# Kernel tuning notes

Hardware: AMD Instinct MI355X
Metric: run time of the kernel (lower is better)

Reference implementation:

```python
import jax, jax.numpy as jnp
import numpy as np

B = 16          # number of point clouds
N_COARSE = 1024  # points per cloud at coarse level
N_FINE = 4096    # points per cloud at fine level
C_IN = 256       # coarse feature channels
C_SKIP = 128     # fine skip feature channels
C_HID = 256
EPS = 1e-16


def setup_inputs() -> dict:
    key = jax.random.key(0)
    ks = jax.random.split(key, 8)
    x = jax.random.normal(ks[0], (B * N_COARSE, C_IN), dtype=jnp.float32)
    pos = jax.random.uniform(ks[1], (B * N_COARSE, 3), dtype=jnp.float32)
    x_skip = jax.random.normal(ks[2], (B * N_FINE, C_SKIP), dtype=jnp.float32)
    pos_skip = jax.random.uniform(ks[3], (B * N_FINE, 3), dtype=jnp.float32)
    # uniform batch assignment (sorted), one segment per cloud
    batch = jnp.repeat(jnp.arange(B, dtype=jnp.int32), N_COARSE)
    batch_skip = jnp.repeat(jnp.arange(B, dtype=jnp.int32), N_FINE)
    # MLP params: Linear(384 -> 256) + ReLU, Linear(256 -> 256) + ReLU
    c0 = C_IN + C_SKIP
    W1 = jax.random.normal(ks[4], (c0, C_HID), dtype=jnp.float32) / np.sqrt(c0)
    b1 = jnp.zeros((C_HID,), dtype=jnp.float32)
    W2 = jax.random.normal(ks[5], (C_HID, C_HID), dtype=jnp.float32) / np.sqrt(C_HID)
    b2 = jnp.zeros((C_HID,), dtype=jnp.float32)
    return {"x": x, "pos": pos, "x_skip": x_skip, "pos_skip": pos_skip,
            "W1": W1, "b1": b1, "W2": W2, "b2": b2,
            "batch": batch, "batch_skip": batch_skip, "k": 3}


def _knn_interpolate(x, pos, pos_skip, k):
    # batch is uniform: reshape into [B, n, ...] blocks (same as per-batch kNN)
    xb = x.reshape(B, N_COARSE, -1)          # [B, Nc, C]
    pc = pos.reshape(B, N_COARSE, 3)         # [B, Nc, 3]
    pf = pos_skip.reshape(B, N_FINE, 3)      # [B, Nf, 3]
    # squared pairwise distances within each cloud: [B, Nf, Nc]
    d2 = jnp.sum((pf[:, :, None, :] - pc[:, None, :, :]) ** 2, axis=-1)
    neg_d2, idx = jax.lax.top_k(-d2, k)      # k nearest -> [B, Nf, k]
    w = 1.0 / jnp.maximum(-neg_d2, EPS)      # inverse-squared-distance weights
    gathered = jax.vmap(lambda xc, i: xc[i])(xb, idx)  # [B, Nf, k, C]
    interp = jnp.sum(w[..., None] * gathered, axis=2) / jnp.sum(w, axis=2, keepdims=True)
    return interp.reshape(B * N_FINE, -1)    # [B*Nf, C]


def reference(x, pos, x_skip, pos_skip, W1, b1, W2, b2, batch, batch_skip, k):
    x_up = _knn_interpolate(x, pos, pos_skip, k)
    h = jnp.concatenate([x_up, x_skip], axis=1)          # [B*Nf, C_IN+C_SKIP]
    h = jax.nn.relu(h @ W1 + b1)
    h = jax.nn.relu(h @ W2 + b2)
    return (h, pos_skip, batch_skip)
```

## Files before the change

### kernel.cpp

```cpp
#include <hip/hip_runtime.h>

#define B_ 16
#define NC 1024
#define NF 4096
#define CIN 256
#define CSKIP 128
#define CHID 256
#define MTOT (B_ * NF)
#define EPS_ 1e-16f

typedef _Float16 f16;
typedef __attribute__((ext_vector_type(8))) _Float16 f16x8;
typedef __attribute__((ext_vector_type(4))) _Float16 f16x4;
typedef __attribute__((ext_vector_type(4))) float f32x4;


__device__ __forceinline__ void gload16(const void* g, void* l)
{
    __builtin_amdgcn_global_load_lds(
        (const __attribute__((address_space(1))) unsigned int*)g,
        (__attribute__((address_space(3))) unsigned int*)l, 16, 0, 0);
}

__global__ __launch_bounds__(256, 4) void misc_kernel(
    const float* __restrict__ x,
    const float* __restrict__ pos, const float* __restrict__ pos_skip,
    const int* __restrict__ batch_skip,
    const float* __restrict__ W1, const float* __restrict__ W2,
    const float* __restrict__ b1,
    int* __restrict__ idx3, float* __restrict__ w3,
    f16* __restrict__ W1bT, f16* __restrict__ W2T, float* __restrict__ b1p,
    f16* __restrict__ y, float* __restrict__ out_tail)
{
    __shared__ __align__(16) char smem[32768];
    const int bid = blockIdx.x;

    if (bid < 256) {
        f16* As = (f16*)smem;
        f16* Bs = (f16*)(smem + 16384);
        const int m0 = (bid >> 1) * 128;
        const int n0 = (bid & 1) * 128;
        const int tid  = threadIdx.x;
        const int lane = tid & 63;
        const int wid  = tid >> 6;
        const int wr   = wid >> 1, wc = wid & 1;
        const int srow = tid >> 1;
        const int scg  = tid & 1;
        const int bn4  = (tid & 31) << 2;
        const int bkb  = (tid >> 5) << 3;

        f32x4 acc[4][4] = {};
        for (int k0 = 0; k0 < 256; k0 += 64) {
            {
                const float* p = x + (size_t)(m0 + srow) * 256 + k0 + scg * 32;
                float v[32];
#pragma unroll
                for (int j = 0; j < 8; ++j) {
                    float4 a = ((const float4*)p)[j];
                    v[j*4+0]=a.x; v[j*4+1]=a.y; v[j*4+2]=a.z; v[j*4+3]=a.w;
                }
#pragma unroll
                for (int j = 0; j < 4; ++j) {
                    f16x8 hh;
#pragma unroll
                    for (int t2 = 0; t2 < 8; ++t2) hh[t2] = (f16)v[j*8+t2];
                    const int sphys = (scg*4 + j) ^ (srow & 7);
                    *(f16x8*)((char*)As + srow*128 + sphys*16) = hh;
                }
            }
#pragma unroll
            for (int c = 0; c < 2; ++c) {
                const int k = bkb + c * 4;
                const float* wp = W1 + (size_t)(k0 + k) * 256 + n0 + bn4;
                float4 r0 = *(const float4*)(wp);
                float4 r1 = *(const float4*)(wp + 256);
                float4 r2 = *(const float4*)(wp + 512);
                float4 r3 = *(const float4*)(wp + 768);
                const int half  = (k >> 2) & 1;
                const int kslot = k >> 3;
                f16x4 t0, t1, t2v, t3;
                t0[0]=(f16)r0.x; t0[1]=(f16)r1.x; t0[2]=(f16)r2.x; t0[3]=(f16)r3.x;
                t1[0]=(f16)r0.y; t1[1]=(f16)r1.y; t1[2]=(f16)r2.y; t1[3]=(f16)r3.y;
                t2v[0]=(f16)r0.z; t2v[1]=(f16)r1.z; t2v[2]=(f16)r2.z; t2v[3]=(f16)r3.z;
                t3[0]=(f16)r0.w; t3[1]=(f16)r1.w; t3[2]=(f16)r2.w; t3[3]=(f16)r3.w;
                *(f16x4*)((char*)Bs + (bn4+0)*128 + ((kslot ^ ((bn4+0)&7))*16) + half*8) = t0;
                *(f16x4*)((char*)Bs + (bn4+1)*128 + ((kslot ^ ((bn4+1)&7))*16) + half*8) = t1;
                *(f16x4*)((char*)Bs + (bn4+2)*128 + ((kslot ^ ((bn4+2)&7))*16) + half*8) = t2v;
                *(f16x4*)((char*)Bs + (bn4+3)*128 + ((kslot ^ ((bn4+3)&7))*16) + half*8) = t3;
            }
            __syncthreads();
#pragma unroll
            for (int h = 0; h < 2; ++h) {
                f16x8 aF[4], bF[4];
#pragma unroll
                for (int m = 0; m < 4; ++m) {
                    const int row  = wr*64 + m*16 + (lane & 15);
                    const int kg   = (h<<2) + (lane>>4);
                    const int slot = kg ^ (row & 7);
                    aF[m] = *(const f16x8*)((const char*)As + row*128 + slot*16);
                }
#pragma unroll
                for (int n = 0; n < 4; ++n) {
                    const int row  = wc*64 + n*16 + (lane & 15);
                    const int kg   = (h<<2) + (lane>>4);
                    const int slot = kg ^ (row & 7);
                    bF[n] = *(const f16x8*)((const char*)Bs + row*128 + slot*16);
                }
#pragma unroll
                for (int m = 0; m < 4; ++m)
#pragma unroll
                    for (int n = 0; n < 4; ++n)
                        acc[m][n] = __builtin_amdgcn_mfma_f32_16x16x32_f16(
                            aF[m], bF[n], acc[m][n], 0, 0, 0);
            }
            __syncthreads();
        }
        const int qq = lane & 15;
#pragma unroll
        for (int m = 0; m < 4; ++m) {
            const int rb = wr*64 + m*16 + ((lane>>4) << 2);
#pragma unroll
            for (int r = 0; r < 4; ++r) {
                const int rg = m0 + rb + r;
                f16x4 hv;
#pragma unroll
                for (int n = 0; n < 4; ++n) hv[n] = (f16)acc[m][n][r];
                *(f16x4*)&y[(size_t)rg * 256 + n0 + wc*64 + qq*4] = hv;
            }
        }
    } else if (bid < 2304) {
        float4* cpos = (float4*)smem;
        float*  cd   = (float*)(smem + 16384);
        int*    ci   = (int*)(smem + 19456);
        const int kb = bid - 256;
        const int b  = kb >> 7;
        const int fb = kb & 127;
        const float* cp = pos + (size_t)b * NC * 3;
        for (int i = threadIdx.x; i < NC; i += 256)
            cpos[i] = make_float4(cp[i*3], cp[i*3+1], cp[i*3+2], 0.0f);
        __syncthreads();

        const int fl = threadIdx.x & 31;
        const int q  = threadIdx.x >> 5;
        const int f  = b * NF + fb * 32 + fl;
        const float px = pos_skip[f*3+0];
        const float py = pos_skip[f*3+1];
        const float pz = pos_skip[f*3+2];

        float d0 = 3.4e38f, d1 = 3.4e38f, d2 = 3.4e38f;
        int   i0 = 0, i1 = 0, i2 = 0;
        const int jbase = q << 7;
#pragma unroll 4
        for (int jj = 0; jj < 128; ++jj) {
            const int j = jbase + jj;
            float4 c = cpos[j];
            float dx = px - c.x, dy = py - c.y, dz = pz - c.z;
            float d = fmaf(dx, dx, fmaf(dy, dy, dz * dz));
            const bool c2 = d < d2, c1 = d < d1, c0 = d < d0;
            d2 = c1 ? d1 : (c2 ? d : d2);  i2 = c1 ? i1 : (c2 ? j : i2);
            d1 = c0 ? d0 : (c1 ? d : d1);  i1 = c0 ? i0 : (c1 ? j : i1);
            d0 = c0 ? d  : d0;             i0 = c0 ? j  : i0;
        }
        const int cb = fl * 24 + q * 3;
        cd[cb+0] = d0; cd[cb+1] = d1; cd[cb+2] = d2;
        ci[cb+0] = i0; ci[cb+1] = i1; ci[cb+2] = i2;
        __syncthreads();

        if (threadIdx.x < 32) {
            float e0 = 3.4e38f, e1 = 3.4e38f, e2 = 3.4e38f;
            int   j0 = 0, j1 = 0, j2 = 0;
#pragma unroll
            for (int s = 0; s < 24; ++s) {
                const float d = cd[fl*24 + s];
                const int   j = ci[fl*24 + s];
                const bool c2 = d < e2, c1 = d < e1, c0 = d < e0;
                e2 = c1 ? e1 : (c2 ? d : e2);  j2 = c1 ? j1 : (c2 ? j : j2);
                e1 = c0 ? e0 : (c1 ? d : e1);  j1 = c0 ? j0 : (c1 ? j : j1);
                e0 = c0 ? d  : e0;             j0 = c0 ? j  : j0;
            }
            const float w0 = 1.0f / fmaxf(e0, EPS_);
            const float w1 = 1.0f / fmaxf(e1, EPS_);
            const float w2 = 1.0f / fmaxf(e2, EPS_);
            const float inv = 1.0f / (w0 + w1 + w2);
            idx3[f*3+0] = b * NC + j0;
            idx3[f*3+1] = b * NC + j1;
            idx3[f*3+2] = b * NC + j2;
            w3[f*3+0] = w0 * inv;
            w3[f*3+1] = w1 * inv;
            w3[f*3+2] = w2 * inv;
        }
    } else if (bid < 2689) {
        const int t = (bid - 2304) * 256 + threadIdx.x;
        if (t < 128 * 256) {
            const int k = t >> 8, n = t & 255;
            W1bT[n * 128 + k] = (f16)W1[(256 + k) * 256 + n];
        } else if (t < 128 * 256 + 256 * 256) {
            const int u = t - 128 * 256;
            const int n = u >> 8, j = u & 255;
            const int k = (j & ~63) + ((j & 3) << 4) + ((j >> 2) & 15);
            W2T[n * 256 + j] = (f16)W2[k * 256 + n];
        } else if (t < 128 * 256 + 256 * 256 + 256) {
            const int j = t - (128 * 256 + 256 * 256);
            const int k = (j & ~63) + ((j & 3) << 4) + ((j >> 2) & 15);
            b1p[j] = b1[k];
        }
    } else {
        const int i = (bid - 2689) * 256 + threadIdx.x;
        const int npos = MTOT * 3;
        if (i < npos)               out_tail[i] = pos_skip[i];
        else if (i < npos + MTOT)   out_tail[i] = (float)batch_skip[i - npos];
    }
}

__global__ __launch_bounds__(256, 2) void fused_gemm12(
    const float* __restrict__ A,
    const f16* __restrict__ B1t,
    const f16* __restrict__ y,
    const int* __restrict__ idx3, const float* __restrict__ w3,
    const float* __restrict__ b1p,
    const f16* __restrict__ B2t,
    const float* __restrict__ b2,
    float* __restrict__ out)
{
    __shared__ __align__(16) char lds[65536];
    f16*  Bs  = (f16*)lds;
    f16*  As  = (f16*)(lds + 32768);
    char* h1s = lds + 32768;

    const int tid  = threadIdx.x;
    const int lane = tid & 63;
    const int wid  = tid >> 6;
    const int wr   = wid >> 1, wc = wid & 1;
    const int m0   = blockIdx.x * 64;

    const int srow_l = lane >> 3;
    const int kch    = (lane & 7) ^ ((lane >> 3) & 7);

    f32x4 acc[2][8] = {};
    for (int k0 = 0; k0 < 128; k0 += 64) {
#pragma unroll
        for (int r = 0; r < 8; ++r) {
            const int c = (wid << 3) + r;
            const int row = (c << 3) + srow_l;
            gload16(B1t + (size_t)row * 128 + k0 + kch * 8, (char*)Bs + (c << 10));
        }
        {
            const int arow = tid >> 2, acg = tid & 3;
            const float* p = A + (size_t)(m0 + arow) * 128 + k0 + acg * 16;
            float v[16];
#pragma unroll
            for (int j = 0; j < 4; ++j) {
                float4 a = ((const float4*)p)[j];
                v[j*4+0]=a.x; v[j*4+1]=a.y; v[j*4+2]=a.z; v[j*4+3]=a.w;
            }
#pragma unroll
            for (int j = 0; j < 2; ++j) {
                f16x8 hh;
#pragma unroll
                for (int t2 = 0; t2 < 8; ++t2) hh[t2] = (f16)v[j*8+t2];
                const int sphys = (acg*2 + j) ^ (arow & 7);
                *(f16x8*)((char*)As + arow*128 + sphys*16) = hh;
            }
        }
        __syncthreads();
#pragma unroll
        for (int h = 0; h < 2; ++h) {
            f16x8 aF[2];
#pragma unroll
            for (int m = 0; m < 2; ++m) {
                const int row  = wr*32 + m*16 + (lane & 15);
                const int kg   = (h<<2) + (lane>>4);
                const int slot = kg ^ (row & 7);
                aF[m] = *(const f16x8*)((const char*)As + row*128 + slot*16);
            }
#pragma unroll
            for (int n = 0; n < 8; ++n) {
                const int row  = wc*128 + n*16 + (lane & 15);
                const int kg   = (h<<2) + (lane>>4);
                const int slot = kg ^ (row & 7);
                f16x8 bF = *(const f16x8*)((const char*)Bs + row*128 + slot*16);
#pragma unroll
                for (int m = 0; m < 2; ++m)
                    acc[m][n] = __builtin_amdgcn_mfma_f32_16x16x32_f16(
                        aF[m], bF, acc[m][n], 0, 0, 0);
            }
        }
        __syncthreads();
    }

    const int qq = lane & 15;
    const f32x4 bv0 = *(const f32x4*)&b1p[wc*128 + qq*4];
    const f32x4 bv1 = *(const f32x4*)&b1p[wc*128 + 64 + qq*4];
#pragma unroll
    for (int m = 0; m < 2; ++m) {
        const int rb = wr*32 + m*16 + ((lane>>4) << 2);
#pragma unroll
        for (int r = 0; r < 4; ++r) {
            const int rl = rb + r;
            const int rg = m0 + rl;
            const int i0 = idx3[rg*3+0], i1 = idx3[rg*3+1], i2 = idx3[rg*3+2];
            const float w0 = w3[rg*3+0], w1 = w3[rg*3+1], w2 = w3[rg*3+2];
#pragma unroll
            for (int g = 0; g < 2; ++g) {
                const int jb = wc*128 + g*64 + qq*4;
                f16x4 y0 = *(const f16x4*)&y[(size_t)i0 * 256 + jb];
                f16x4 y1 = *(const f16x4*)&y[(size_t)i1 * 256 + jb];
                f16x4 y2 = *(const f16x4*)&y[(size_t)i2 * 256 + jb];
                const f32x4 bv = g ? bv1 : bv0;
                f16x4 hv;
#pragma unroll
                for (int n = 0; n < 4; ++n) {
                    float v = acc[m][g*4+n][r]
                            + w0*(float)y0[n] + w1*(float)y1[n] + w2*(float)y2[n]
                            + bv[n];
                    hv[n] = (f16)fmaxf(v, 0.0f);
                }
                const int slot = jb >> 3;
                const int phys = (slot & ~7) | ((slot & 7) ^ (rl & 7));
                *(f16x4*)(h1s + rl*512 + phys*16 + ((jb >> 2) & 1) * 8) = hv;
            }
        }
    }
    __syncthreads();

    f32x4 acc2[2][8] = {};
    for (int k0 = 0; k0 < 256; k0 += 64) {
#pragma unroll
        for (int r = 0; r < 8; ++r) {
            const int c = (wid << 3) + r;
            const int row = (c << 3) + srow_l;
            gload16(B2t + (size_t)row * 256 + k0 + kch * 8, (char*)Bs + (c << 10));
        }
        __syncthreads();
#pragma unroll
        for (int h = 0; h < 2; ++h) {
            f16x8 aF[2];
#pragma unroll
            for (int m = 0; m < 2; ++m) {
                const int row   = wr*32 + m*16 + (lane & 15);
                const int kg    = (h<<2) + (lane>>4);
                const int aslot = (k0 >> 3) + (kg ^ (row & 7));
                aF[m] = *(const f16x8*)(h1s + row*512 + aslot*16);
            }
#pragma unroll
            for (int n = 0; n < 8; ++n) {
                const int row  = wc*128 + n*16 + (lane & 15);
                const int kg   = (h<<2) + (lane>>4);
                const int slot = kg ^ (row & 7);
                f16x8 bF = *(const f16x8*)((const char*)Bs + row*128 + slot*16);
#pragma unroll
                for (int m = 0; m < 2; ++m)
                    acc2[m][n] = __builtin_amdgcn_mfma_f32_16x16x32_f16(
                        aF[m], bF, acc2[m][n], 0, 0, 0);
            }
        }
        __syncthreads();
    }

#pragma unroll
    for (int m = 0; m < 2; ++m) {
#pragma unroll
        for (int n = 0; n < 8; ++n) {
            const int col = wc*128 + n*16 + (lane & 15);
            const float bv = b2[col];
#pragma unroll
            for (int r = 0; r < 4; ++r) {
                const int row = m0 + wr*32 + m*16 + ((lane>>4) << 2) + r;
                out[(size_t)row * 256 + col] = fmaxf(acc2[m][n][r] + bv, 0.0f);
            }
        }
    }
}

extern "C" void kernel_launch(void* const* d_in, const int* in_sizes, int n_in,
                              void* d_out, int out_size, void* d_ws, size_t ws_size,
                              hipStream_t stream)
{
    const float* x        = (const float*)d_in[0];
    const float* pos      = (const float*)d_in[1];
    const float* x_skip   = (const float*)d_in[2];
    const float* pos_skip = (const float*)d_in[3];
    const float* W1       = (const float*)d_in[4];
    const float* b1       = (const float*)d_in[5];
    const float* W2       = (const float*)d_in[6];
    const float* b2       = (const float*)d_in[7];
    const int*   batch_skip = (const int*)d_in[9];
    float* out = (float*)d_out;

    char* ws = (char*)d_ws;
    int*   idx3 = (int*)ws;
    float* w3   = (float*)(ws + (1u << 20));
    f16*   W1bT = (f16*)(ws + (2u << 20));
    f16*   W2T  = (f16*)(ws + (2u << 20) + (256u << 10));
    float* b1p  = (float*)(ws + (2u << 20) + (512u << 10));
    f16*   y    = (f16*)(ws + (4u << 20));

    misc_kernel<<<3713, 256, 0, stream>>>(
        x, pos, pos_skip, batch_skip, W1, W2, b1,
        idx3, w3, W1bT, W2T, b1p, y, out + (size_t)MTOT * CHID);

    fused_gemm12<<<MTOT / 64, 256, 0, stream>>>(
        x_skip, W1bT, y, idx3, w3, b1p, W2T, b2, out);
}
```

Measured before the change: 177.7 us.

## Move kNN search into the fused GEMM kernel and keep indices/weights in LDS

The kNN search leaves the preprocessing kernel and now runs at the start of each 64-row GEMM block. Four threads per fine point each scan 256 coarse points, and their partial top-3 lists are merged with wave shuffles. Indices and weights stay in LDS, so the idx3/w3 global round trip and 2048 blocks of work in the first kernel go away. In exchange the GEMM kernel does serial distance work before its MFMA phase, and LDS use grows slightly past 64KB, which may lower occupancy.

```diff
diff --git a/kernel.cpp b/kernel.cpp
--- a/kernel.cpp
+++ b/kernel.cpp
@@ -24,11 +24,9 @@
 
 __global__ __launch_bounds__(256, 4) void misc_kernel(
     const float* __restrict__ x,
-    const float* __restrict__ pos, const float* __restrict__ pos_skip,
-    const int* __restrict__ batch_skip,
+    const float* __restrict__ pos_skip, const int* __restrict__ batch_skip,
     const float* __restrict__ W1, const float* __restrict__ W2,
     const float* __restrict__ b1,
-    int* __restrict__ idx3, float* __restrict__ w3,
     f16* __restrict__ W1bT, f16* __restrict__ W2T, float* __restrict__ b1p,
     f16* __restrict__ y, float* __restrict__ out_tail)
 {
@@ -128,69 +126,8 @@
                 *(f16x4*)&y[(size_t)rg * 256 + n0 + wc*64 + qq*4] = hv;
             }
         }
-    } else if (bid < 2304) {
-        float4* cpos = (float4*)smem;
-        float*  cd   = (float*)(smem + 16384);
-        int*    ci   = (int*)(smem + 19456);
-        const int kb = bid - 256;
-        const int b  = kb >> 7;
-        const int fb = kb & 127;
-        const float* cp = pos + (size_t)b * NC * 3;
-        for (int i = threadIdx.x; i < NC; i += 256)
-            cpos[i] = make_float4(cp[i*3], cp[i*3+1], cp[i*3+2], 0.0f);
-        __syncthreads();
-
-        const int fl = threadIdx.x & 31;
-        const int q  = threadIdx.x >> 5;
-        const int f  = b * NF + fb * 32 + fl;
-        const float px = pos_skip[f*3+0];
-        const float py = pos_skip[f*3+1];
-        const float pz = pos_skip[f*3+2];
-
-        float d0 = 3.4e38f, d1 = 3.4e38f, d2 = 3.4e38f;
-        int   i0 = 0, i1 = 0, i2 = 0;
-        const int jbase = q << 7;
-#pragma unroll 4
-        for (int jj = 0; jj < 128; ++jj) {
-            const int j = jbase + jj;
-            float4 c = cpos[j];
-            float dx = px - c.x, dy = py - c.y, dz = pz - c.z;
-            float d = fmaf(dx, dx, fmaf(dy, dy, dz * dz));
-            const bool c2 = d < d2, c1 = d < d1, c0 = d < d0;
-            d2 = c1 ? d1 : (c2 ? d : d2);  i2 = c1 ? i1 : (c2 ? j : i2);
-            d1 = c0 ? d0 : (c1 ? d : d1);  i1 = c0 ? i0 : (c1 ? j : i1);
-            d0 = c0 ? d  : d0;             i0 = c0 ? j  : i0;
-        }
-        const int cb = fl * 24 + q * 3;
-        cd[cb+0] = d0; cd[cb+1] = d1; cd[cb+2] = d2;
-        ci[cb+0] = i0; ci[cb+1] = i1; ci[cb+2] = i2;
-        __syncthreads();
-
-        if (threadIdx.x < 32) {
-            float e0 = 3.4e38f, e1 = 3.4e38f, e2 = 3.4e38f;
-            int   j0 = 0, j1 = 0, j2 = 0;
-#pragma unroll
-            for (int s = 0; s < 24; ++s) {
-                const float d = cd[fl*24 + s];
-                const int   j = ci[fl*24 + s];
-                const bool c2 = d < e2, c1 = d < e1, c0 = d < e0;
-                e2 = c1 ? e1 : (c2 ? d : e2);  j2 = c1 ? j1 : (c2 ? j : j2);
-                e1 = c0 ? e0 : (c1 ? d : e1);  j1 = c0 ? j0 : (c1 ? j : j1);
-                e0 = c0 ? d  : e0;             j0 = c0 ? j  : j0;
-            }
-            const float w0 = 1.0f / fmaxf(e0, EPS_);
-            const float w1 = 1.0f / fmaxf(e1, EPS_);
-            const float w2 = 1.0f / fmaxf(e2, EPS_);
-            const float inv = 1.0f / (w0 + w1 + w2);
-            idx3[f*3+0] = b * NC + j0;
-            idx3[f*3+1] = b * NC + j1;
-            idx3[f*3+2] = b * NC + j2;
-            w3[f*3+0] = w0 * inv;
-            w3[f*3+1] = w1 * inv;
-            w3[f*3+2] = w2 * inv;
-        }
-    } else if (bid < 2689) {
-        const int t = (bid - 2304) * 256 + threadIdx.x;
+    } else if (bid < 641) {
+        const int t = (bid - 256) * 256 + threadIdx.x;
         if (t < 128 * 256) {
             const int k = t >> 8, n = t & 255;
             W1bT[n * 128 + k] = (f16)W1[(256 + k) * 256 + n];
@@ -205,33 +142,89 @@
             b1p[j] = b1[k];
         }
     } else {
-        const int i = (bid - 2689) * 256 + threadIdx.x;
+        const int i = (bid - 641) * 256 + threadIdx.x;
         const int npos = MTOT * 3;
         if (i < npos)               out_tail[i] = pos_skip[i];
         else if (i < npos + MTOT)   out_tail[i] = (float)batch_skip[i - npos];
     }
 }
 
-__global__ __launch_bounds__(256, 2) void fused_gemm12(
+__global__ __launch_bounds__(256, 2) void fused_all(
+    const float* __restrict__ pos, const float* __restrict__ pos_skip,
     const float* __restrict__ A,
     const f16* __restrict__ B1t,
     const f16* __restrict__ y,
-    const int* __restrict__ idx3, const float* __restrict__ w3,
     const float* __restrict__ b1p,
     const f16* __restrict__ B2t,
     const float* __restrict__ b2,
     float* __restrict__ out)
 {
-    __shared__ __align__(16) char lds[65536];
-    f16*  Bs  = (f16*)lds;
-    f16*  As  = (f16*)(lds + 32768);
-    char* h1s = lds + 32768;
+    __shared__ __align__(16) char lds[67072];
+    f16*   Bs  = (f16*)lds;
+    f16*   As  = (f16*)(lds + 32768);
+    char*  h1s = lds + 32768;
+    int*   kni = (int*)(lds + 65536);
+    float* knw = (float*)(lds + 65536 + 768);
 
     const int tid  = threadIdx.x;
     const int lane = tid & 63;
     const int wid  = tid >> 6;
     const int wr   = wid >> 1, wc = wid & 1;
     const int m0   = blockIdx.x * 64;
+    const int bat  = m0 >> 12;
+
+    {
+        float4* cpos = (float4*)(lds + 32768);
+        const float* cp = pos + (size_t)(bat << 10) * 3;
+        for (int i = tid; i < NC; i += 256)
+            cpos[i] = make_float4(cp[i*3], cp[i*3+1], cp[i*3+2], 0.0f);
+        __syncthreads();
+
+        const int fl = tid >> 2;
+        const int q  = tid & 3;
+        const int f  = m0 + fl;
+        const float px = pos_skip[f*3+0];
+        const float py = pos_skip[f*3+1];
+        const float pz = pos_skip[f*3+2];
+
+        float d0 = 3.4e38f, d1 = 3.4e38f, d2 = 3.4e38f;
+        int   i0 = 0, i1 = 0, i2 = 0;
+        const int jb = q << 8;
+#pragma unroll 4
+        for (int jj = 0; jj < 256; ++jj) {
+            const int j = jb + jj;
+            float4 c = cpos[j];
+            float dx = px - c.x, dy = py - c.y, dz = pz - c.z;
+            float d = fmaf(dx, dx, fmaf(dy, dy, dz * dz));
+            const bool c2 = d < d2, c1 = d < d1, c0 = d < d0;
+            d2 = c1 ? d1 : (c2 ? d : d2);  i2 = c1 ? i1 : (c2 ? j : i2);
+            d1 = c0 ? d0 : (c1 ? d : d1);  i1 = c0 ? i0 : (c1 ? j : i1);
+            d0 = c0 ? d  : d0;             i0 = c0 ? j  : i0;
+        }
+#pragma unroll
+        for (int st = 1; st <= 2; st <<= 1) {
+            float e0 = __shfl_xor(d0, st, 64), e1 = __shfl_xor(d1, st, 64), e2 = __shfl_xor(d2, st, 64);
+            int   g0 = __shfl_xor(i0, st, 64), g1 = __shfl_xor(i1, st, 64), g2 = __shfl_xor(i2, st, 64);
+#pragma unroll
+            for (int s = 0; s < 3; ++s) {
+                const float d = s == 0 ? e0 : (s == 1 ? e1 : e2);
+                const int   j = s == 0 ? g0 : (s == 1 ? g1 : g2);
+                const bool c2 = d < d2, c1 = d < d1, c0 = d < d0;
+                d2 = c1 ? d1 : (c2 ? d : d2);  i2 = c1 ? i1 : (c2 ? j : i2);
+                d1 = c0 ? d0 : (c1 ? d : d1);  i1 = c0 ? i0 : (c1 ? j : i1);
+                d0 = c0 ? d  : d0;             i0 = c0 ? j  : i0;
+            }
+        }
+        if (q == 0) {
+            const float w0 = 1.0f / fmaxf(d0, EPS_);
+            const float w1 = 1.0f / fmaxf(d1, EPS_);
+            const float w2 = 1.0f / fmaxf(d2, EPS_);
+            const float inv = 1.0f / (w0 + w1 + w2);
+            kni[fl*3+0] = i0; kni[fl*3+1] = i1; kni[fl*3+2] = i2;
+            knw[fl*3+0] = w0 * inv; knw[fl*3+1] = w1 * inv; knw[fl*3+2] = w2 * inv;
+        }
+        __syncthreads();
+    }
 
     const int srow_l = lane >> 3;
     const int kch    = (lane & 7) ^ ((lane >> 3) & 7);
@@ -288,7 +281,8 @@
         __syncthreads();
     }
 
-    const int qq = lane & 15;
+    const int qq  = lane & 15;
+    const int gb  = bat << 10;
     const f32x4 bv0 = *(const f32x4*)&b1p[wc*128 + qq*4];
     const f32x4 bv1 = *(const f32x4*)&b1p[wc*128 + 64 + qq*4];
 #pragma unroll
@@ -297,15 +291,16 @@
 #pragma unroll
         for (int r = 0; r < 4; ++r) {
             const int rl = rb + r;
-            const int rg = m0 + rl;
-            const int i0 = idx3[rg*3+0], i1 = idx3[rg*3+1], i2 = idx3[rg*3+2];
-            const float w0 = w3[rg*3+0], w1 = w3[rg*3+1], w2 = w3[rg*3+2];
+            const int i0 = gb + kni[rl*3+0];
+            const int i1 = gb + kni[rl*3+1];
+            const int i2 = gb + kni[rl*3+2];
+            const float w0 = knw[rl*3+0], w1 = knw[rl*3+1], w2 = knw[rl*3+2];
 #pragma unroll
             for (int g = 0; g < 2; ++g) {
-                const int jb = wc*128 + g*64 + qq*4;
-                f16x4 y0 = *(const f16x4*)&y[(size_t)i0 * 256 + jb];
-                f16x4 y1 = *(const f16x4*)&y[(size_t)i1 * 256 + jb];
-                f16x4 y2 = *(const f16x4*)&y[(size_t)i2 * 256 + jb];
+                const int jb2 = wc*128 + g*64 + qq*4;
+                f16x4 y0 = *(const f16x4*)&y[(size_t)i0 * 256 + jb2];
+                f16x4 y1 = *(const f16x4*)&y[(size_t)i1 * 256 + jb2];
+                f16x4 y2 = *(const f16x4*)&y[(size_t)i2 * 256 + jb2];
                 const f32x4 bv = g ? bv1 : bv0;
                 f16x4 hv;
 #pragma unroll
@@ -315,9 +310,9 @@
                             + bv[n];
                     hv[n] = (f16)fmaxf(v, 0.0f);
                 }
-                const int slot = jb >> 3;
+                const int slot = jb2 >> 3;
                 const int phys = (slot & ~7) | ((slot & 7) ^ (rl & 7));
-                *(f16x4*)(h1s + rl*512 + phys*16 + ((jb >> 2) & 1) * 8) = hv;
+                *(f16x4*)(h1s + rl*512 + phys*16 + ((jb2 >> 2) & 1) * 8) = hv;
             }
         }
     }
@@ -388,17 +383,15 @@
     float* out = (float*)d_out;
 
     char* ws = (char*)d_ws;
-    int*   idx3 = (int*)ws;
-    float* w3   = (float*)(ws + (1u << 20));
-    f16*   W1bT = (f16*)(ws + (2u << 20));
-    f16*   W2T  = (f16*)(ws + (2u << 20) + (256u << 10));
-    float* b1p  = (float*)(ws + (2u << 20) + (512u << 10));
-    f16*   y    = (f16*)(ws + (4u << 20));
-
-    misc_kernel<<<3713, 256, 0, stream>>>(
-        x, pos, pos_skip, batch_skip, W1, W2, b1,
-        idx3, w3, W1bT, W2T, b1p, y, out + (size_t)MTOT * CHID);
-
-    fused_gemm12<<<MTOT / 64, 256, 0, stream>>>(
-        x_skip, W1bT, y, idx3, w3, b1p, W2T, b2, out);
+    f16*   W1bT = (f16*)ws;
+    f16*   W2T  = (f16*)(ws + (256u << 10));
+    float* b1p  = (float*)(ws + (512u << 10));
+    f16*   y    = (f16*)(ws + (1u << 20));
+
+    misc_kernel<<<1665, 256, 0, stream>>>(
+        x, pos_skip, batch_skip, W1, W2, b1,
+        W1bT, W2T, b1p, y, out + (size_t)MTOT * CHID);
+
+    fused_all<<<MTOT / 64, 256, 0, stream>>>(
+        pos, pos_skip, x_skip, W1bT, y, b1p, W2T, b2, out);
 }
```

After: 208.1 us. +17.1%, slower.
